# Performance work log

Hardware: AMD Instinct MI355X
Metric: run time of the kernel (lower is better)

The kernel has to match this reference:

```python
import jax, jax.numpy as jnp
import numpy as np
import math

B, S, D, H = 2, 2048, 2048, 16
DH = D // H  # 128


def _rope(x, cos, sin):
    # x: [b, s, h, dh]; cos/sin: [s, dh//2]
    b, s, h, dh = x.shape
    x2 = x.reshape(b, s, h, dh // 2, 2)
    a, bb = x2[..., 0], x2[..., 1]
    c = cos[None, :, None, :]
    sn = sin[None, :, None, :]
    out = jnp.stack([a * c - bb * sn, a * sn + bb * c], axis=-1)
    return out.reshape(b, s, h, dh)


def setup_inputs() -> dict:
    key = jax.random.key(0)
    ks = jax.random.split(key, 6)
    x = jax.random.normal(ks[0], (B, S, D), dtype=jnp.float32)
    # RoPE frequencies (theta=10000) as cos/sin of shape [S, DH//2]
    inv_freq = 1.0 / (10000.0 ** (np.arange(0, DH, 2, dtype=np.float32) / DH))
    t = np.arange(S, dtype=np.float32)
    ang = jnp.asarray(np.outer(t, inv_freq))  # [S, DH//2]
    freqs_cos = jnp.cos(ang)
    freqs_sin = jnp.sin(ang)
    # causal additive mask [1,1,S,S]
    neg = jnp.finfo(jnp.float32).min
    mask = jnp.where(jnp.tril(jnp.ones((S, S), dtype=bool)), 0.0, neg)[None, None]
    sc = 0.02
    wq = jax.random.normal(ks[1], (D, D), dtype=jnp.float32) * sc
    wk = jax.random.normal(ks[2], (D, D), dtype=jnp.float32) * sc
    wv = jax.random.normal(ks[3], (D, D), dtype=jnp.float32) * sc
    wo = jax.random.normal(ks[4], (D, D), dtype=jnp.float32) * sc
    return {"x": x, "freqs_cos": freqs_cos, "freqs_sin": freqs_sin,
            "mask": mask, "wq": wq, "wk": wk, "wv": wv, "wo": wo}


def reference(x, freqs_cos, freqs_sin, mask, wq, wk, wv, wo):
    b, s, _ = x.shape
    # torch Linear: y = x @ W.T (weights stored [out, in])
    xq = (x @ wq.T).reshape(b, s, H, DH)
    xk = (x @ wk.T).reshape(b, s, H, DH)
    xv = (x @ wv.T).reshape(b, s, H, DH)
    xq = _rope(xq, freqs_cos, freqs_sin)
    xk = _rope(xk, freqs_cos, freqs_sin)
    # [b, h, s, dh]
    q = xq.transpose(0, 2, 1, 3)
    k = xk.transpose(0, 2, 1, 3)
    v = xv.transpose(0, 2, 1, 3)
    scores = jnp.einsum('bhqd,bhkd->bhqk', q, k) / math.sqrt(DH)
    scores = scores + mask
    attn = jax.nn.softmax(scores, axis=-1)  # dropout p=0 (eval)
    out = jnp.einsum('bhqk,bhkd->bhqd', attn, v)
    out = out.transpose(0, 2, 1, 3).reshape(b, s, D)
    return out @ wo.T
```

## Files before the change

### kernel.cpp

```cpp
#include <hip/hip_runtime.h>

#define B_ 2
#define S_ 2048
#define D_ 2048
#define H_ 16
#define DH_ 128

typedef __bf16 bf16_8 __attribute__((ext_vector_type(8)));
typedef __bf16 bf16_4 __attribute__((ext_vector_type(4)));
typedef float f32x4 __attribute__((ext_vector_type(4)));

__device__ __forceinline__ f32x4 mfma16(bf16_8 a, bf16_8 b, f32x4 c) {
  return __builtin_amdgcn_mfma_f32_16x16x32_bf16(a, b, c, 0, 0, 0);
}

__device__ __forceinline__ bf16_8 load8(const float* p) {
  f32x4 a = *(const f32x4*)p;
  f32x4 b = *(const f32x4*)(p + 4);
  bf16_8 r;
  r[0] = (__bf16)a[0]; r[1] = (__bf16)a[1]; r[2] = (__bf16)a[2]; r[3] = (__bf16)a[3];
  r[4] = (__bf16)b[0]; r[5] = (__bf16)b[1]; r[6] = (__bf16)b[2]; r[7] = (__bf16)b[3];
  return r;
}

__device__ __forceinline__ void async16(const __bf16* g, __bf16* l) {
  __builtin_amdgcn_global_load_lds(
      (const __attribute__((address_space(1))) void*)g,
      (__attribute__((address_space(3))) void*)l, 16, 0, 0);
}

__global__ __launch_bounds__(256) void cvt_all(
    const float* __restrict__ x, const float* __restrict__ wq,
    const float* __restrict__ wk, const float* __restrict__ wv,
    const float* __restrict__ wo, __bf16* __restrict__ xb,
    __bf16* __restrict__ wqb, __bf16* __restrict__ wkb,
    __bf16* __restrict__ wvb, __bf16* __restrict__ wob)
{
  const int W8 = (D_ * D_) / 8;
  int i = blockIdx.x * 256 + threadIdx.x;
  if (i < 2 * W8) {
    *(bf16_8*)(xb + (size_t)i * 8) = load8(x + (size_t)i * 8);
  } else {
    int j = i - 2 * W8;
    int sel = j >> 19, off = j & (W8 - 1);
    const float* s = sel == 0 ? wq : sel == 1 ? wk : sel == 2 ? wv : wo;
    __bf16* d = sel == 0 ? wqb : sel == 1 ? wkb : sel == 2 ? wvb : wob;
    *(bf16_8*)(d + (size_t)off * 8) = load8(s + (size_t)off * 8);
  }
}

template <bool WB>
__global__ __launch_bounds__(256) void qkv_gemm(
    const __bf16* __restrict__ A,
    const float* __restrict__ wqf, const float* __restrict__ wkf,
    const float* __restrict__ wvf,
    const __bf16* __restrict__ wqb, const __bf16* __restrict__ wkb,
    const __bf16* __restrict__ wvb,
    const float* __restrict__ fc, const float* __restrict__ fs,
    __bf16* __restrict__ Qo, __bf16* __restrict__ Ko, __bf16* __restrict__ Vo)
{
  constexpr int TILE = 128 * 32;
  constexpr int STAGE_ELEMS = WB ? 4 * TILE : (128 * 32 + 128 * 40);
  constexpr int TS_ELEMS = 64 * 136;
  constexpr int SM_ELEMS = STAGE_ELEMS > TS_ELEMS ? STAGE_ELEMS : TS_ELEMS;
  __shared__ __align__(16) __bf16 smem[SM_ELEMS];

  const int tid = threadIdx.x;
  const int wave = tid >> 6, lane = tid & 63;
  const int quad = lane >> 4, l16 = lane & 15;
  const int m0 = blockIdx.y * 128, n0 = blockIdx.x * 128;
  const int wsel = n0 >> 11, nloc = n0 & 2047;
  const int wm = (wave >> 1) * 64, wn = (wave & 1) * 64;
  const __bf16* agl = A + (size_t)(m0 + wave * 32 + (lane >> 2)) * 2048 + (lane & 3) * 8;
  f32x4 acc[4][4] = {};
  if (WB) {
    const __bf16* Wb = wsel == 0 ? wqb : wsel == 1 ? wkb : wvb;
    const __bf16* wgl = Wb + (size_t)(nloc + wave * 32 + (lane >> 2)) * 2048 + (lane & 3) * 8;
    auto STAGE = [&](int k0, int p) {
      __bf16* ab = smem + p * TILE + (wave * 32) * 32;
      __bf16* wb2 = smem + 2 * TILE + p * TILE + (wave * 32) * 32;
      async16(agl + k0,             ab);
      async16(agl + 16 * 2048 + k0, ab + 16 * 32);
      async16(wgl + k0,             wb2);
      async16(wgl + 16 * 2048 + k0, wb2 + 16 * 32);
    };
    STAGE(0, 0);
#pragma unroll 2
    for (int it = 0; it < 64; ++it) {
      const int p = it & 1;
      if (it + 1 < 64) {
        STAGE((it + 1) * 32, p ^ 1);
        asm volatile("s_waitcnt vmcnt(4)" ::: "memory");
      } else {
        asm volatile("s_waitcnt vmcnt(0)" ::: "memory");
      }
      __builtin_amdgcn_s_barrier();
      asm volatile("" ::: "memory");
      const __bf16* Ab = smem + p * TILE;
      const __bf16* Wbuf = smem + 2 * TILE + p * TILE;
      bf16_8 af[4], bfr[4];
      for (int i = 0; i < 4; ++i) {
        af[i]  = *(const bf16_8*)(Ab   + (wm + i * 16 + l16) * 32 + quad * 8);
        bfr[i] = *(const bf16_8*)(Wbuf + (wn + i * 16 + l16) * 32 + quad * 8);
      }
      for (int mi = 0; mi < 4; ++mi)
        for (int ni = 0; ni < 4; ++ni)
          acc[mi][ni] = mfma16(af[mi], bfr[ni], acc[mi][ni]);
      asm volatile("s_waitcnt lgkmcnt(0)" ::: "memory");
      __builtin_amdgcn_s_barrier();
      asm volatile("" ::: "memory");
    }
  } else {
    auto As = (__bf16(*)[32])smem;
    auto Ws = (__bf16(*)[40])(smem + 128 * 32);
    const float* W = wsel == 0 ? wqf : wsel == 1 ? wkf : wvf;
    const int srow = tid >> 1, scol = (tid & 1) * 16;
    const float* wg = W + (size_t)(nloc + srow) * 2048 + scol;
    for (int k0 = 0; k0 < 2048; k0 += 32) {
      __syncthreads();
      async16(agl + k0,             &As[wave * 32][0]);
      async16(agl + 16 * 2048 + k0, &As[wave * 32 + 16][0]);
      *(bf16_8*)&Ws[srow][scol]     = load8(wg + k0);
      *(bf16_8*)&Ws[srow][scol + 8] = load8(wg + k0 + 8);
      __syncthreads();
      bf16_8 af[4], bfr[4];
      for (int i = 0; i < 4; ++i) {
        af[i]  = *(const bf16_8*)&As[wm + i * 16 + l16][quad * 8];
        bfr[i] = *(const bf16_8*)&Ws[wn + i * 16 + l16][quad * 8];
      }
      for (int mi = 0; mi < 4; ++mi)
        for (int ni = 0; ni < 4; ++ni)
          acc[mi][ni] = mfma16(af[mi], bfr[ni], acc[mi][ni]);
    }
  }
  if (wsel < 2) {
    const float qscale = wsel == 0 ? 0.08838834764831845f * 1.4426950408889634f
                                   : 1.0f;
    __bf16* O = wsel == 0 ? Qo : Ko;
    for (int mi = 0; mi < 4; ++mi)
      for (int ni = 0; ni < 4; ++ni)
        for (int r = 0; r < 4; ++r) {
          int row = m0 + wm + mi * 16 + quad * 4 + r;
          int col = nloc + wn + ni * 16 + l16;
          float self = acc[mi][ni][r];
          float oth = __shfl_xor(self, 1);
          int s = row & (S_ - 1);
          int dh = col & (DH_ - 1);
          float c = fc[s * (DH_ / 2) + (dh >> 1)];
          float sn = fs[s * (DH_ / 2) + (dh >> 1)];
          float o = (dh & 1) ? (oth * sn + self * c) : (self * c - oth * sn);
          O[(size_t)row * 2048 + col] = (__bf16)(o * qscale);
        }
  } else {
    auto Ts = (__bf16(*)[136])smem;
    const int b = m0 >> 11, h = nloc >> 7;
    __bf16* vb = Vo + ((size_t)(b * H_ + h) * DH_) * S_ + (m0 & (S_ - 1));
    for (int p = 0; p < 2; ++p) {
      __syncthreads();
      if ((wn >> 6) == p) {
        for (int mi = 0; mi < 4; ++mi)
          for (int ni = 0; ni < 4; ++ni) {
            int cl = ni * 16 + l16;
            int rl = wm + mi * 16 + quad * 4;
            bf16_4 pk;
            for (int r = 0; r < 4; ++r) pk[r] = (__bf16)acc[mi][ni][r];
            *(bf16_4*)&Ts[cl][rl] = pk;
          }
      }
      __syncthreads();
      for (int i = 0; i < 4; ++i) {
        int dh = p * 64 + i * 16 + (tid >> 4);
        int sc = (tid & 15) * 8;
        *(bf16_8*)(vb + (size_t)dh * S_ + sc) = *(const bf16_8*)&Ts[dh - p * 64][sc];
      }
    }
  }
}

template <bool WB>
__global__ __launch_bounds__(256) void out_gemm(
    const __bf16* __restrict__ A, const float* __restrict__ Wf,
    const __bf16* __restrict__ Wb, float* __restrict__ C)
{
  constexpr int TILE = 128 * 32;
  constexpr int SM_ELEMS = WB ? 4 * TILE : (128 * 32 + 128 * 40);
  __shared__ __align__(16) __bf16 smem[SM_ELEMS];
  const int tid = threadIdx.x;
  const int wave = tid >> 6, lane = tid & 63;
  const int quad = lane >> 4, l16 = lane & 15;
  const int m0 = blockIdx.y * 128, n0 = blockIdx.x * 128;
  const int wm = (wave >> 1) * 64, wn = (wave & 1) * 64;
  const __bf16* agl = A + (size_t)(m0 + wave * 32 + (lane >> 2)) * 2048 + (lane & 3) * 8;
  f32x4 acc[4][4] = {};
  if (WB) {
    const __bf16* wgl = Wb + (size_t)(n0 + wave * 32 + (lane >> 2)) * 2048 + (lane & 3) * 8;
    auto STAGE = [&](int k0, int p) {
      __bf16* ab = smem + p * TILE + (wave * 32) * 32;
      __bf16* wb2 = smem + 2 * TILE + p * TILE + (wave * 32) * 32;
      async16(agl + k0,             ab);
      async16(agl + 16 * 2048 + k0, ab + 16 * 32);
      async16(wgl + k0,             wb2);
      async16(wgl + 16 * 2048 + k0, wb2 + 16 * 32);
    };
    STAGE(0, 0);
#pragma unroll 2
    for (int it = 0; it < 64; ++it) {
      const int p = it & 1;
      if (it + 1 < 64) {
        STAGE((it + 1) * 32, p ^ 1);
        asm volatile("s_waitcnt vmcnt(4)" ::: "memory");
      } else {
        asm volatile("s_waitcnt vmcnt(0)" ::: "memory");
      }
      __builtin_amdgcn_s_barrier();
      asm volatile("" ::: "memory");
      const __bf16* Ab = smem + p * TILE;
      const __bf16* Wbuf = smem + 2 * TILE + p * TILE;
      bf16_8 af[4], bfr[4];
      for (int i = 0; i < 4; ++i) {
        af[i]  = *(const bf16_8*)(Ab   + (wm + i * 16 + l16) * 32 + quad * 8);
        bfr[i] = *(const bf16_8*)(Wbuf + (wn + i * 16 + l16) * 32 + quad * 8);
      }
      for (int mi = 0; mi < 4; ++mi)
        for (int ni = 0; ni < 4; ++ni)
          acc[mi][ni] = mfma16(af[mi], bfr[ni], acc[mi][ni]);
      asm volatile("s_waitcnt lgkmcnt(0)" ::: "memory");
      __builtin_amdgcn_s_barrier();
      asm volatile("" ::: "memory");
    }
  } else {
    auto As = (__bf16(*)[32])smem;
    auto Ws = (__bf16(*)[40])(smem + 128 * 32);
    const int srow = tid >> 1, scol = (tid & 1) * 16;
    const float* wg = Wf + (size_t)(n0 + srow) * 2048 + scol;
    for (int k0 = 0; k0 < 2048; k0 += 32) {
      __syncthreads();
      async16(agl + k0,             &As[wave * 32][0]);
      async16(agl + 16 * 2048 + k0, &As[wave * 32 + 16][0]);
      *(bf16_8*)&Ws[srow][scol]     = load8(wg + k0);
      *(bf16_8*)&Ws[srow][scol + 8] = load8(wg + k0 + 8);
      __syncthreads();
      bf16_8 af[4], bfr[4];
      for (int i = 0; i < 4; ++i) {
        af[i]  = *(const bf16_8*)&As[wm + i * 16 + l16][quad * 8];
        bfr[i] = *(const bf16_8*)&Ws[wn + i * 16 + l16][quad * 8];
      }
      for (int mi = 0; mi < 4; ++mi)
        for (int ni = 0; ni < 4; ++ni)
          acc[mi][ni] = mfma16(af[mi], bfr[ni], acc[mi][ni]);
    }
  }
  for (int mi = 0; mi < 4; ++mi)
    for (int ni = 0; ni < 4; ++ni)
      for (int r = 0; r < 4; ++r) {
        int row = m0 + wm + mi * 16 + quad * 4 + r;
        int col = n0 + wn + ni * 16 + l16;
        C[(size_t)row * 2048 + col] = acc[mi][ni][r];
      }
}

__global__ __launch_bounds__(256) void attn_kernel(
    const __bf16* __restrict__ Q, const __bf16* __restrict__ K,
    const __bf16* __restrict__ Vt_g, __bf16* __restrict__ O)
{
  __shared__ __bf16 Ks[2][64 * 128];
  __shared__ __bf16 Vt[128 * 64];
  __shared__ __bf16 Ps[4][32][72];
  const int tid = threadIdx.x;
  const int wave = tid >> 6, lane = tid & 63;
  const int quad = lane >> 4, l16 = lane & 15;
  const int qt = gridDim.x - 1 - blockIdx.x;
  const int bh = blockIdx.y;
  const size_t base = (size_t)(bh >> 4) * S_ * D_ + (size_t)(bh & 15) * DH_;
  const size_t vtb = (size_t)bh * DH_ * S_;
  const int q0 = qt * 128;
  const int wmin = q0 + wave * 32;

  bf16_8 qf[2][4];
  for (int qs = 0; qs < 2; ++qs) {
    int qrow = wmin + qs * 16 + l16;
    for (int kk = 0; kk < 4; ++kk)
      qf[qs][kk] = *(const bf16_8*)(Q + base + (size_t)qrow * D_ + kk * 32 + quad * 8);
  }
  asm volatile("s_waitcnt vmcnt(0)" ::: "memory");

  const int krs = wave * 4 + (lane >> 4);
  const __bf16* kgl = K + base + (size_t)krs * D_ + ((lane & 15) ^ krs) * 8;
  const int vrs = wave * 8 + (lane >> 3);
  const __bf16* vgl = Vt_g + vtb + (size_t)vrs * S_ + ((lane & 7) ^ (lane >> 3)) * 8;

  f32x4 oacc[2][8] = {};
  float lsum[2][4] = {};
  const int nt = 2 * qt + 2;

  for (int p = 0; p < 4; ++p)
    async16(kgl + (size_t)(p * 16) * D_, Ks[0] + (p * 16 + wave * 4) * 128);
  for (int p = 0; p < 4; ++p)
    async16(vgl + (size_t)(p * 32) * S_, Vt + (p * 32 + wave * 8) * 64);

  int cur = 0;
  for (int kt = 0; kt < nt; ++kt) {
    const bool more = (kt + 1 < nt);
    if (more) {
      for (int p = 0; p < 4; ++p)
        async16(kgl + (size_t)((kt + 1) * 64 + p * 16) * D_,
                Ks[cur ^ 1] + (p * 16 + wave * 4) * 128);
      asm volatile("s_waitcnt vmcnt(8)" ::: "memory");
    } else {
      asm volatile("s_waitcnt vmcnt(4)" ::: "memory");
    }
    __builtin_amdgcn_s_barrier();
    asm volatile("" ::: "memory");

    const bool active = (kt * 64 <= wmin + 31);
    if (active) {
      const bool diag = (kt * 64 + 63 > wmin);
      const __bf16* ksb = Ks[cur];
      for (int n = 0; n < 4; ++n) {
        f32x4 s0 = {}, s1 = {};
        __builtin_amdgcn_s_setprio(1);
#pragma unroll
        for (int kk = 0; kk < 4; ++kk) {
          bf16_8 kf = *(const bf16_8*)&ksb[(n * 16 + l16) * 128 + (((kk * 4 + quad) ^ l16) * 8)];
          s0 = mfma16(qf[0][kk], kf, s0);
          s1 = mfma16(qf[1][kk], kf, s1);
        }
        __builtin_amdgcn_s_setprio(0);
#pragma unroll
        for (int qs = 0; qs < 2; ++qs) {
          f32x4 sv = qs ? s1 : s0;
          for (int r = 0; r < 4; ++r) {
            float v = sv[r];
            if (diag) {
              int qr = wmin + qs * 16 + quad * 4 + r;
              if (kt * 64 + n * 16 + l16 > qr) v = -INFINITY;
            }
            float p = exp2f(v);
            lsum[qs][r] += p;
            Ps[wave][qs * 16 + quad * 4 + r][n * 16 + l16] = (__bf16)p;
          }
        }
      }
    }

    if (more) asm volatile("s_waitcnt vmcnt(4)" ::: "memory");
    else      asm volatile("s_waitcnt vmcnt(0)" ::: "memory");
    __builtin_amdgcn_s_barrier();
    asm volatile("" ::: "memory");

    if (active) {
      bf16_8 pf0[2], pf1[2];
      for (int qs = 0; qs < 2; ++qs) {
        pf0[qs] = *(const bf16_8*)&Ps[wave][qs * 16 + l16][quad * 8];
        pf1[qs] = *(const bf16_8*)&Ps[wave][qs * 16 + l16][32 + quad * 8];
      }
      __builtin_amdgcn_s_setprio(1);
#pragma unroll
      for (int nc = 0; nc < 8; ++nc) {
        bf16_8 vf0 = *(const bf16_8*)&Vt[(nc * 16 + l16) * 64 + ((quad ^ (l16 & 7)) * 8)];
        bf16_8 vf1 = *(const bf16_8*)&Vt[(nc * 16 + l16) * 64 + (((quad + 4) ^ (l16 & 7)) * 8)];
        oacc[0][nc] = mfma16(pf0[0], vf0, oacc[0][nc]);
        oacc[0][nc] = mfma16(pf1[0], vf1, oacc[0][nc]);
        oacc[1][nc] = mfma16(pf0[1], vf0, oacc[1][nc]);
        oacc[1][nc] = mfma16(pf1[1], vf1, oacc[1][nc]);
      }
      __builtin_amdgcn_s_setprio(0);
    }

    asm volatile("s_waitcnt lgkmcnt(0)" ::: "memory");
    __builtin_amdgcn_s_barrier();
    asm volatile("" ::: "memory");
    if (more)
      for (int p = 0; p < 4; ++p)
        async16(vgl + (size_t)(p * 32) * S_ + (size_t)(kt + 1) * 64,
                Vt + (p * 32 + wave * 8) * 64);
    cur ^= 1;
  }

  for (int qs = 0; qs < 2; ++qs)
    for (int r = 0; r < 4; ++r) {
      float l = lsum[qs][r];
      l += __shfl_xor(l, 1);
      l += __shfl_xor(l, 2);
      l += __shfl_xor(l, 4);
      l += __shfl_xor(l, 8);
      float rinv = 1.f / l;
      int qr = wmin + qs * 16 + quad * 4 + r;
      for (int nc = 0; nc < 8; ++nc)
        O[base + (size_t)qr * D_ + nc * 16 + l16] = (__bf16)(oacc[qs][nc][r] * rinv);
    }
}

extern "C" void kernel_launch(void* const* d_in, const int* in_sizes, int n_in,
                              void* d_out, int out_size, void* d_ws, size_t ws_size,
                              hipStream_t stream)
{
  const float* x    = (const float*)d_in[0];
  const float* fcos = (const float*)d_in[1];
  const float* fsin = (const float*)d_in[2];
  const float* wq   = (const float*)d_in[4];
  const float* wk   = (const float*)d_in[5];
  const float* wv   = (const float*)d_in[6];
  const float* wo   = (const float*)d_in[7];
  float* out = (float*)d_out;

  const size_t T = (size_t)B_ * S_ * D_;
  const size_t W = (size_t)D_ * D_;
  __bf16* xb  = (__bf16*)d_ws;
  __bf16* qw  = xb + T;
  __bf16* kw  = qw + T;
  __bf16* vt  = kw + T;
  __bf16* wqb = vt + T;
  __bf16* wkb = wqb + W;
  __bf16* wvb = wkb + W;
  __bf16* wob = wvb + W;
  __bf16* ow  = xb;

  const bool wb = ws_size >= (4 * T + 4 * W) * sizeof(__bf16);
  const int W8 = (int)(W / 8);
  cvt_all<<<(wb ? 6 : 2) * W8 / 256, 256, 0, stream>>>(
      x, wq, wk, wv, wo, xb, wqb, wkb, wvb, wob);
  if (wb)
    qkv_gemm<true><<<dim3(48, 32), 256, 0, stream>>>(
        xb, nullptr, nullptr, nullptr, wqb, wkb, wvb, fcos, fsin, qw, kw, vt);
  else
    qkv_gemm<false><<<dim3(48, 32), 256, 0, stream>>>(
        xb, wq, wk, wv, nullptr, nullptr, nullptr, fcos, fsin, qw, kw, vt);
  attn_kernel<<<dim3(S_ / 128, B_ * H_), 256, 0, stream>>>(qw, kw, vt, ow);
  if (wb)
    out_gemm<true><<<dim3(16, 32), 256, 0, stream>>>(ow, nullptr, wob, out);
  else
    out_gemm<false><<<dim3(16, 32), 256, 0, stream>>>(ow, wo, nullptr, out);
}
```

Before: 439.7 us.

## Load V fragments directly from global into registers, dropping LDS staging

Removes the shared-memory V tile and its async copy. Each wave now loads its own V fragments straight from global memory at the start of each key tile, so the latency overlaps the QK^T and softmax work. This also removes the mid-iteration barrier and simplifies the vmcnt accounting to cover only the K prefetch. In exchange, every wave fetches the same V tile, giving four times the global and L2 traffic for V, and holding 16 bf16x8 V fragments in registers raises VGPR pressure and may lower occupancy.

```diff
diff --git a/kernel.cpp b/kernel.cpp
--- a/kernel.cpp
+++ b/kernel.cpp
@@ -264,7 +264,6 @@
     const __bf16* __restrict__ Vt_g, __bf16* __restrict__ O)
 {
   __shared__ __bf16 Ks[2][64 * 128];
-  __shared__ __bf16 Vt[128 * 64];
   __shared__ __bf16 Ps[4][32][72];
   const int tid = threadIdx.x;
   const int wave = tid >> 6, lane = tid & 63;
@@ -286,8 +285,7 @@
 
   const int krs = wave * 4 + (lane >> 4);
   const __bf16* kgl = K + base + (size_t)krs * D_ + ((lane & 15) ^ krs) * 8;
-  const int vrs = wave * 8 + (lane >> 3);
-  const __bf16* vgl = Vt_g + vtb + (size_t)vrs * S_ + ((lane & 7) ^ (lane >> 3)) * 8;
+  const __bf16* vdir = Vt_g + vtb + (size_t)l16 * S_ + quad * 8;
 
   f32x4 oacc[2][8] = {};
   float lsum[2][4] = {};
@@ -295,8 +293,6 @@
 
   for (int p = 0; p < 4; ++p)
     async16(kgl + (size_t)(p * 16) * D_, Ks[0] + (p * 16 + wave * 4) * 128);
-  for (int p = 0; p < 4; ++p)
-    async16(vgl + (size_t)(p * 32) * S_, Vt + (p * 32 + wave * 8) * 64);
 
   int cur = 0;
   for (int kt = 0; kt < nt; ++kt) {
@@ -305,15 +301,23 @@
       for (int p = 0; p < 4; ++p)
         async16(kgl + (size_t)((kt + 1) * 64 + p * 16) * D_,
                 Ks[cur ^ 1] + (p * 16 + wave * 4) * 128);
-      asm volatile("s_waitcnt vmcnt(8)" ::: "memory");
+      asm volatile("s_waitcnt vmcnt(4)" ::: "memory");
     } else {
-      asm volatile("s_waitcnt vmcnt(4)" ::: "memory");
+      asm volatile("s_waitcnt vmcnt(0)" ::: "memory");
     }
     __builtin_amdgcn_s_barrier();
     asm volatile("" ::: "memory");
 
     const bool active = (kt * 64 <= wmin + 31);
     if (active) {
+      bf16_8 vf0[8], vf1[8];
+#pragma unroll
+      for (int nc = 0; nc < 8; ++nc) {
+        const __bf16* vp = vdir + (size_t)(nc * 16) * S_ + kt * 64;
+        vf0[nc] = *(const bf16_8*)vp;
+        vf1[nc] = *(const bf16_8*)(vp + 32);
+      }
+
       const bool diag = (kt * 64 + 63 > wmin);
       const __bf16* ksb = Ks[cur];
       for (int n = 0; n < 4; ++n) {
@@ -341,14 +345,7 @@
           }
         }
       }
-    }
-
-    if (more) asm volatile("s_waitcnt vmcnt(4)" ::: "memory");
-    else      asm volatile("s_waitcnt vmcnt(0)" ::: "memory");
-    __builtin_amdgcn_s_barrier();
-    asm volatile("" ::: "memory");
-
-    if (active) {
+
       bf16_8 pf0[2], pf1[2];
       for (int qs = 0; qs < 2; ++qs) {
         pf0[qs] = *(const bf16_8*)&Ps[wave][qs * 16 + l16][quad * 8];
@@ -357,12 +354,10 @@
       __builtin_amdgcn_s_setprio(1);
 #pragma unroll
       for (int nc = 0; nc < 8; ++nc) {
-        bf16_8 vf0 = *(const bf16_8*)&Vt[(nc * 16 + l16) * 64 + ((quad ^ (l16 & 7)) * 8)];
-        bf16_8 vf1 = *(const bf16_8*)&Vt[(nc * 16 + l16) * 64 + (((quad + 4) ^ (l16 & 7)) * 8)];
-        oacc[0][nc] = mfma16(pf0[0], vf0, oacc[0][nc]);
-        oacc[0][nc] = mfma16(pf1[0], vf1, oacc[0][nc]);
-        oacc[1][nc] = mfma16(pf0[1], vf0, oacc[1][nc]);
-        oacc[1][nc] = mfma16(pf1[1], vf1, oacc[1][nc]);
+        oacc[0][nc] = mfma16(pf0[0], vf0[nc], oacc[0][nc]);
+        oacc[0][nc] = mfma16(pf1[0], vf1[nc], oacc[0][nc]);
+        oacc[1][nc] = mfma16(pf0[1], vf0[nc], oacc[1][nc]);
+        oacc[1][nc] = mfma16(pf1[1], vf1[nc], oacc[1][nc]);
       }
       __builtin_amdgcn_s_setprio(0);
     }
@@ -370,10 +365,6 @@
     asm volatile("s_waitcnt lgkmcnt(0)" ::: "memory");
     __builtin_amdgcn_s_barrier();
     asm volatile("" ::: "memory");
-    if (more)
-      for (int p = 0; p < 4; ++p)
-        async16(vgl + (size_t)(p * 32) * S_ + (size_t)(kt + 1) * 64,
-                Vt + (p * 32 + wave * 8) * 64);
     cur ^= 1;
   }
 
```

New measurement: 602.4 us. +37.0%, slower.
